# Kernel tuning notes

Hardware: AMD Instinct MI355X
Metric: run time of the kernel (lower is better)

## Reference

```python
import jax, jax.numpy as jnp
import numpy as np

NUM_QUBITS = 6
DIM = 2 ** NUM_QUBITS  # 64


def _u_gate(theta, phi, lam):
    # qiskit U(theta, phi, lam)
    c = jnp.cos(theta / 2).astype(jnp.complex64)
    s = jnp.sin(theta / 2).astype(jnp.complex64)
    ephi = jnp.exp(1j * phi.astype(jnp.complex64))
    elam = jnp.exp(1j * lam.astype(jnp.complex64))
    return jnp.stack([
        jnp.stack([c, -elam * s]),
        jnp.stack([ephi * s, ephi * elam * c]),
    ])


def _p_gate(lam):
    one = jnp.ones((), jnp.complex64)
    return jnp.stack([
        jnp.stack([one, jnp.zeros((), jnp.complex64)]),
        jnp.stack([jnp.zeros((), jnp.complex64), jnp.exp(1j * lam.astype(jnp.complex64))]),
    ])


def _controlled(U):
    # 4x4 matrix in |control, target> basis: block-diag(I2, U)
    return jnp.eye(4, dtype=jnp.complex64).at[2:, 2:].set(U)


_CX = jnp.array([[1, 0, 0, 0], [0, 1, 0, 0], [0, 0, 0, 1], [0, 0, 1, 0]], dtype=jnp.complex64)


def _apply_1q(psi, U, q):
    # psi: (B, 2,2,2,2,2,2); qubit q (qiskit little-endian) -> axis 6-q
    ax = NUM_QUBITS - q
    psi = jnp.moveaxis(psi, ax, -1)
    psi = psi @ U.T
    return jnp.moveaxis(psi, -1, ax)


def _apply_2q(psi, G, qa, qb):
    # G is 4x4 acting on (qa, qb) with index 2*bit(qa)+bit(qb)
    a, b = NUM_QUBITS - qa, NUM_QUBITS - qb
    psi = jnp.moveaxis(psi, (a, b), (-2, -1))
    shp = psi.shape
    psi = (psi.reshape(shp[:-2] + (4,)) @ G.T).reshape(shp)
    return jnp.moveaxis(psi, (-2, -1), (a, b))


def _circuit(features, params):
    # amplitude encoding (qc.initialize with L2 normalization; |0> fallback for zero vec)
    norm = jnp.linalg.norm(features, axis=1, keepdims=True)
    safe = jnp.where(jnp.isclose(norm, 0.0), 1.0, norm)
    e0 = jnp.zeros((1, DIM), features.dtype).at[0, 0].set(1.0)
    psi = jnp.where(jnp.isclose(norm, 0.0), e0, features / safe)
    psi = psi.astype(jnp.complex64).reshape((-1,) + (2,) * NUM_QUBITS)

    def U3(i):
        return _u_gate(params[i], params[i + 1], params[i + 2])

    # layer 1: U on all qubits (params 0..17)
    for q in range(NUM_QUBITS):
        psi = _apply_1q(psi, U3(3 * q), q)
    # cx(2,1); p(18,1); cx(4,3); p(19,3)
    psi = _apply_2q(psi, _CX, 2, 1)
    psi = _apply_1q(psi, _p_gate(params[18]), 1)
    psi = _apply_2q(psi, _CX, 4, 3)
    psi = _apply_1q(psi, _p_gate(params[19]), 3)
    # layer 2: U on [0,1,3,5] (params 20..31)
    idx = 20
    for q in [0, 1, 3, 5]:
        psi = _apply_1q(psi, U3(idx), q)
        idx += 3
    # controlled-U(32..34) ctrl 0 -> tgt 1; controlled-U(35..37) ctrl 3 -> tgt 5
    psi = _apply_2q(psi, _controlled(U3(32)), 0, 1)
    psi = _apply_2q(psi, _controlled(U3(35)), 3, 5)
    # cx(3,1); p(38,1)
    psi = _apply_2q(psi, _CX, 3, 1)
    psi = _apply_1q(psi, _p_gate(params[38]), 1)
    # final: U on [0,1] (39..44); CU(45..47) ctrl 0 -> tgt 1; U on [0,1] (48..53)
    psi = _apply_1q(psi, U3(39), 0)
    psi = _apply_1q(psi, U3(42), 1)
    psi = _apply_2q(psi, _controlled(U3(45)), 0, 1)
    psi = _apply_1q(psi, U3(48), 0)
    psi = _apply_1q(psi, U3(51), 1)

    # observable kron(diag(1,-1), I_32): +1 for index < 32, -1 otherwise (Z on qubit 5)
    probs = jnp.abs(psi.reshape(-1, DIM)) ** 2
    sign = jnp.where(jnp.arange(DIM) < DIM // 2, 1.0, -1.0).astype(jnp.float32)
    return (probs @ sign).astype(jnp.float32)


def setup_inputs() -> dict:
    key = jax.random.key(0)
    kf, kp = jax.random.split(key)
    features = jax.random.normal(kf, (262144, 64), dtype=jnp.float32)
    params = jax.random.uniform(kp, (54,), dtype=jnp.float32) * (0.1 * np.pi)
    return {"features": features, "params": params}


def reference(features, params):
    return _circuit(features, params)
```

## Files before the change

### kernel.cpp

```cpp
#include <hip/hip_runtime.h>
#include <hip/hip_bf16.h>

using f32x4  = __attribute__((ext_vector_type(4))) float;
using bf16x8 = __attribute__((ext_vector_type(8))) short;

__device__ __attribute__((aligned(16))) unsigned short g_Abf[64 * 64];
__device__ float2 g_U[64 * 64];
__device__ float  g_A00;

__device__ inline unsigned short f2bf(float x) {
  unsigned u = __builtin_bit_cast(unsigned, x);
  return (unsigned short)((u + 0x7FFFu + ((u >> 16) & 1u)) >> 16);
}
__device__ inline float2 cmul(float2 a, float2 b) {
  return make_float2(a.x * b.x - a.y * b.y, a.x * b.y + a.y * b.x);
}
__device__ inline float2 cadd(float2 a, float2 b) { return make_float2(a.x + b.x, a.y + b.y); }

__device__ inline void gate1q(float2* psi, int t, int sub, int q,
                              float2 u00, float2 u01, float2 u10, float2 u11) {
  const int bit = 1 << q, mask = bit - 1;
#pragma unroll
  for (int pp = 0; pp < 8; ++pp) {
    int p  = sub * 8 + pp;
    int i0 = ((p & ~mask) << 1) | (p & mask);
    int i1 = i0 | bit;
    float2 a0 = psi[i0 * 64 + t], a1 = psi[i1 * 64 + t];
    psi[i0 * 64 + t] = cadd(cmul(u00, a0), cmul(u01, a1));
    psi[i1 * 64 + t] = cadd(cmul(u10, a0), cmul(u11, a1));
  }
}

__device__ inline void gatec(float2* psi, int t, int sub, int c, int g,
                             float2 v00, float2 v01, float2 v10, float2 v11) {
  const int cb = 1 << c, gb = 1 << g;
  const int lo = (c < g ? c : g), hi = (c < g ? g : c);
  const int mlo = (1 << lo) - 1, mhi = (1 << hi) - 1;
#pragma unroll
  for (int pp = 0; pp < 4; ++pp) {
    int p = sub * 4 + pp;
    int y = ((p & ~mlo) << 1) | (p & mlo);
    y     = ((y & ~mhi) << 1) | (y & mhi);
    int i0 = y | cb;
    int i1 = i0 | gb;
    float2 a0 = psi[i0 * 64 + t], a1 = psi[i1 * 64 + t];
    psi[i0 * 64 + t] = cadd(cmul(v00, a0), cmul(v01, a1));
    psi[i1 * 64 + t] = cadd(cmul(v10, a0), cmul(v11, a1));
  }
}

__global__ __launch_bounds__(256) void sim_kernel(const float* __restrict__ P) {
  __shared__ float2 psi[64 * 64];
  __shared__ float tS[54], tC[54], tSh[54], tCh[54];
  const int t = threadIdx.x & 63, sub = threadIdx.x >> 6;
  if (threadIdx.x < 54) {
    float p = P[threadIdx.x];
    tS[threadIdx.x]  = __sinf(p);
    tC[threadIdx.x]  = __cosf(p);
    tSh[threadIdx.x] = __sinf(0.5f * p);
    tCh[threadIdx.x] = __cosf(0.5f * p);
  }
  for (int idx = threadIdx.x; idx < 4096; idx += 256)
    psi[idx] = make_float2(((idx >> 6) == (idx & 63)) ? 1.f : 0.f, 0.f);
  __syncthreads();

  float2 u00, u01, u10, u11;
  const float2 Z = make_float2(0.f, 0.f), ONE = make_float2(1.f, 0.f);
  auto U3L = [&](int i) {
    float ch = tCh[i], sh = tSh[i];
    float cp = tC[i + 1], sp = tS[i + 1];
    float cl = tC[i + 2], sl = tS[i + 2];
    u00 = make_float2(ch, 0.f);
    u01 = make_float2(-cl * sh, -sl * sh);
    u10 = make_float2(cp * sh, sp * sh);
    u11 = make_float2((cp * cl - sp * sl) * ch, (cp * sl + sp * cl) * ch);
  };
  auto PH = [&](int i) { return make_float2(tC[i], tS[i]); };

#pragma unroll
  for (int q = 0; q < 6; ++q) {
    U3L(3 * q);
    gate1q(psi, t, sub, q, u00, u01, u10, u11);
    __syncthreads();
  }
  gatec(psi, t, sub, 2, 1, Z, ONE, ONE, Z); __syncthreads();
  gate1q(psi, t, sub, 1, ONE, Z, Z, PH(18)); __syncthreads();
  gatec(psi, t, sub, 4, 3, Z, ONE, ONE, Z); __syncthreads();
  gate1q(psi, t, sub, 3, ONE, Z, Z, PH(19)); __syncthreads();
  const int qs[4] = {0, 1, 3, 5};
#pragma unroll
  for (int ii = 0; ii < 4; ++ii) {
    U3L(20 + 3 * ii);
    gate1q(psi, t, sub, qs[ii], u00, u01, u10, u11);
    __syncthreads();
  }
  U3L(32); gatec(psi, t, sub, 0, 1, u00, u01, u10, u11); __syncthreads();
  U3L(35); gatec(psi, t, sub, 3, 5, u00, u01, u10, u11); __syncthreads();
  gatec(psi, t, sub, 3, 1, Z, ONE, ONE, Z); __syncthreads();
  gate1q(psi, t, sub, 1, ONE, Z, Z, PH(38)); __syncthreads();
  U3L(39); gate1q(psi, t, sub, 0, u00, u01, u10, u11); __syncthreads();
  U3L(42); gate1q(psi, t, sub, 1, u00, u01, u10, u11); __syncthreads();
  U3L(45); gatec(psi, t, sub, 0, 1, u00, u01, u10, u11); __syncthreads();
  U3L(48); gate1q(psi, t, sub, 0, u00, u01, u10, u11); __syncthreads();
  U3L(51); gate1q(psi, t, sub, 1, u00, u01, u10, u11); __syncthreads();
  for (int idx = threadIdx.x; idx < 4096; idx += 256) g_U[idx] = psi[idx];
}

__global__ __launch_bounds__(256) void amat_kernel() {
  const int idx = blockIdx.x * 256 + threadIdx.x;
  const int j = idx >> 6, k = idx & 63;
  float s = 0.f;
#pragma unroll 8
  for (int i = 0; i < 64; ++i) {
    float2 uj = g_U[i * 64 + j], uk = g_U[i * 64 + k];
    float d = uj.x * uk.x + uj.y * uk.y;
    s += (i < 32) ? d : -d;
  }
  g_Abf[idx] = f2bf(s);
  if (idx == 0) g_A00 = s;
}

#define MFMA(A, B, C) __builtin_amdgcn_mfma_f32_16x16x32_bf16(A, B, C, 0, 0, 0)

__global__ __launch_bounds__(256) void qexp_kernel(const float* __restrict__ F, float* __restrict__ out) {
  __shared__ float flds[4][16 * 68];
  const int lane = threadIdx.x & 63;
  const int wid  = threadIdx.x >> 6;
  const int g = lane >> 4, c0 = lane & 15;
  float* fl = flds[wid];

  const unsigned short* ab = g_Abf + (unsigned)(c0 * 64 + g * 8);
  const bf16x8 b00 = *(const bf16x8*)(ab);
  const bf16x8 b01 = *(const bf16x8*)(ab + 32);
  const bf16x8 b10 = *(const bf16x8*)(ab + 16 * 64);
  const bf16x8 b11 = *(const bf16x8*)(ab + 16 * 64 + 32);
  const bf16x8 b20 = *(const bf16x8*)(ab + 32 * 64);
  const bf16x8 b21 = *(const bf16x8*)(ab + 32 * 64 + 32);
  const bf16x8 b30 = *(const bf16x8*)(ab + 48 * 64);
  const bf16x8 b31 = *(const bf16x8*)(ab + 48 * 64 + 32);
  const float A00 = g_A00;

  const int nwaves = gridDim.x << 2;
  for (int tile = (int)(blockIdx.x << 2) | wid; tile < 16384; tile += nwaves) {
    const int b0 = tile << 4;
    const float* fr = F + (size_t)(b0 + c0) * 64 + g * 8;
    const float4 v0 = *(const float4*)(fr);
    const float4 v1 = *(const float4*)(fr + 4);
    const float4 v2 = *(const float4*)(fr + 32);
    const float4 v3 = *(const float4*)(fr + 36);
    bf16x8 a0, a1;
    a0[0] = f2bf(v0.x); a0[1] = f2bf(v0.y); a0[2] = f2bf(v0.z); a0[3] = f2bf(v0.w);
    a0[4] = f2bf(v1.x); a0[5] = f2bf(v1.y); a0[6] = f2bf(v1.z); a0[7] = f2bf(v1.w);
    a1[0] = f2bf(v2.x); a1[1] = f2bf(v2.y); a1[2] = f2bf(v2.z); a1[3] = f2bf(v2.w);
    a1[4] = f2bf(v3.x); a1[5] = f2bf(v3.y); a1[6] = f2bf(v3.z); a1[7] = f2bf(v3.w);
    float* fw = fl + c0 * 68 + g * 8;
    *(float4*)(fw)      = v0;
    *(float4*)(fw + 4)  = v1;
    *(float4*)(fw + 32) = v2;
    *(float4*)(fw + 36) = v3;

    f32x4 acc0 = {0.f, 0.f, 0.f, 0.f}, acc1 = acc0, acc2 = acc0, acc3 = acc0;
    acc0 = MFMA(a0, b00, acc0); acc0 = MFMA(a1, b01, acc0);
    acc1 = MFMA(a0, b10, acc1); acc1 = MFMA(a1, b11, acc1);
    acc2 = MFMA(a0, b20, acc2); acc2 = MFMA(a1, b21, acc2);
    acc3 = MFMA(a0, b30, acc3); acc3 = MFMA(a1, b31, acc3);

    asm volatile("s_waitcnt lgkmcnt(0)" ::: "memory");
    float num0 = 0, num1 = 0, num2 = 0, num3 = 0, den0 = 0, den1 = 0, den2 = 0, den3 = 0;
    const float* fb = fl + g * 4 * 68 + c0;
#define EPI(ACC, NT) { \
    float fv0 = fb[(NT) * 16];          num0 = fmaf(ACC[0], fv0, num0); den0 = fmaf(fv0, fv0, den0); \
    float fv1 = fb[68 + (NT) * 16];     num1 = fmaf(ACC[1], fv1, num1); den1 = fmaf(fv1, fv1, den1); \
    float fv2 = fb[2 * 68 + (NT) * 16]; num2 = fmaf(ACC[2], fv2, num2); den2 = fmaf(fv2, fv2, den2); \
    float fv3 = fb[3 * 68 + (NT) * 16]; num3 = fmaf(ACC[3], fv3, num3); den3 = fmaf(fv3, fv3, den3); }
    EPI(acc0, 0) EPI(acc1, 1) EPI(acc2, 2) EPI(acc3, 3)
#undef EPI
#pragma unroll
    for (int m = 1; m < 16; m <<= 1) {
      num0 += __shfl_xor(num0, m, 64); den0 += __shfl_xor(den0, m, 64);
      num1 += __shfl_xor(num1, m, 64); den1 += __shfl_xor(den1, m, 64);
      num2 += __shfl_xor(num2, m, 64); den2 += __shfl_xor(den2, m, 64);
      num3 += __shfl_xor(num3, m, 64); den3 += __shfl_xor(den3, m, 64);
    }
    if (c0 < 4) {
      float nv = (c0 == 0) ? num0 : (c0 == 1) ? num1 : (c0 == 2) ? num2 : num3;
      float dv = (c0 == 0) ? den0 : (c0 == 1) ? den1 : (c0 == 2) ? den2 : den3;
      out[b0 + g * 4 + c0] = (dv <= 1e-16f) ? A00 : nv / dv;
    }
  }
}

extern "C" void kernel_launch(void* const* d_in, const int* in_sizes, int n_in,
                              void* d_out, int out_size, void* d_ws, size_t ws_size,
                              hipStream_t stream) {
  const float* F = (const float*)d_in[0];
  const float* P = (const float*)d_in[1];
  float* out = (float*)d_out;
  sim_kernel<<<1, 256, 0, stream>>>(P);
  amat_kernel<<<16, 256, 0, stream>>>();
  qexp_kernel<<<2048, 256, 0, stream>>>(F, out);
}
```

Measured before the change: 121.4 us.

## Fuse circuit simulation into expectation kernel, redundantly per block, using psi=Ux GEMM

Merges the three launches into one kernel. Every block re-simulates the 64x64 circuit unitary in shared memory and builds a bf16 stacked real/imag matrix of U. Each row is then handled as psi = U x via eight MFMA tiles, with the signed probability sum normalised by the total norm, instead of a quadratic form against a precomputed A matrix. A double-buffered register prefetch of feature tiles is added over 16 tiles per wave. This removes two launches and the global round trip, but each of 256 blocks repeats the serial gate simulation and the MFMA work per row doubles.

```diff
diff --git a/kernel.cpp b/kernel.cpp
--- a/kernel.cpp
+++ b/kernel.cpp
@@ -1,12 +1,7 @@
 #include <hip/hip_runtime.h>
-#include <hip/hip_bf16.h>
 
 using f32x4  = __attribute__((ext_vector_type(4))) float;
 using bf16x8 = __attribute__((ext_vector_type(8))) short;
-
-__device__ __attribute__((aligned(16))) unsigned short g_Abf[64 * 64];
-__device__ float2 g_U[64 * 64];
-__device__ float  g_A00;
 
 __device__ inline unsigned short f2bf(float x) {
   unsigned u = __builtin_bit_cast(unsigned, x);
@@ -49,18 +44,27 @@
   }
 }
 
-__global__ __launch_bounds__(256) void sim_kernel(const float* __restrict__ P) {
+#define MFMA(A, B, C) __builtin_amdgcn_mfma_f32_16x16x32_bf16(A, B, C, 0, 0, 0)
+
+__global__ __launch_bounds__(256) void qfused(const float* __restrict__ F,
+                                              const float* __restrict__ Pp,
+                                              float* __restrict__ out) {
   __shared__ float2 psi[64 * 64];
+  __shared__ __attribute__((aligned(16))) unsigned short Plds[128 * 64];
   __shared__ float tS[54], tC[54], tSh[54], tCh[54];
-  const int t = threadIdx.x & 63, sub = threadIdx.x >> 6;
-  if (threadIdx.x < 54) {
-    float p = P[threadIdx.x];
-    tS[threadIdx.x]  = __sinf(p);
-    tC[threadIdx.x]  = __cosf(p);
-    tSh[threadIdx.x] = __sinf(0.5f * p);
-    tCh[threadIdx.x] = __cosf(0.5f * p);
+  __shared__ float sA00;
+
+  const int tid = threadIdx.x;
+  const int t = tid & 63, sub = tid >> 6;
+
+  if (tid < 54) {
+    float p = Pp[tid];
+    tS[tid]  = __sinf(p);
+    tC[tid]  = __cosf(p);
+    tSh[tid] = __sinf(0.5f * p);
+    tCh[tid] = __cosf(0.5f * p);
   }
-  for (int idx = threadIdx.x; idx < 4096; idx += 256)
+  for (int idx = tid; idx < 4096; idx += 256)
     psi[idx] = make_float2(((idx >> 6) == (idx & 63)) ? 1.f : 0.f, 0.f);
   __syncthreads();
 
@@ -79,9 +83,7 @@
 
 #pragma unroll
   for (int q = 0; q < 6; ++q) {
-    U3L(3 * q);
-    gate1q(psi, t, sub, q, u00, u01, u10, u11);
-    __syncthreads();
+    U3L(3 * q); gate1q(psi, t, sub, q, u00, u01, u10, u11); __syncthreads();
   }
   gatec(psi, t, sub, 2, 1, Z, ONE, ONE, Z); __syncthreads();
   gate1q(psi, t, sub, 1, ONE, Z, Z, PH(18)); __syncthreads();
@@ -90,9 +92,7 @@
   const int qs[4] = {0, 1, 3, 5};
 #pragma unroll
   for (int ii = 0; ii < 4; ++ii) {
-    U3L(20 + 3 * ii);
-    gate1q(psi, t, sub, qs[ii], u00, u01, u10, u11);
-    __syncthreads();
+    U3L(20 + 3 * ii); gate1q(psi, t, sub, qs[ii], u00, u01, u10, u11); __syncthreads();
   }
   U3L(32); gatec(psi, t, sub, 0, 1, u00, u01, u10, u11); __syncthreads();
   U3L(35); gatec(psi, t, sub, 3, 5, u00, u01, u10, u11); __syncthreads();
@@ -103,91 +103,89 @@
   U3L(45); gatec(psi, t, sub, 0, 1, u00, u01, u10, u11); __syncthreads();
   U3L(48); gate1q(psi, t, sub, 0, u00, u01, u10, u11); __syncthreads();
   U3L(51); gate1q(psi, t, sub, 1, u00, u01, u10, u11); __syncthreads();
-  for (int idx = threadIdx.x; idx < 4096; idx += 256) g_U[idx] = psi[idx];
-}
 
-__global__ __launch_bounds__(256) void amat_kernel() {
-  const int idx = blockIdx.x * 256 + threadIdx.x;
-  const int j = idx >> 6, k = idx & 63;
-  float s = 0.f;
-#pragma unroll 8
-  for (int i = 0; i < 64; ++i) {
-    float2 uj = g_U[i * 64 + j], uk = g_U[i * 64 + k];
-    float d = uj.x * uk.x + uj.y * uk.y;
-    s += (i < 32) ? d : -d;
+  if (tid < 64) {
+    float2 v = psi[tid * 64];
+    float term = (v.x * v.x + v.y * v.y) * (tid < 32 ? 1.f : -1.f);
+#pragma unroll
+    for (int m = 1; m < 64; m <<= 1) term += __shfl_xor(term, m, 64);
+    if (tid == 0) sA00 = term;
   }
-  g_Abf[idx] = f2bf(s);
-  if (idx == 0) g_A00 = s;
-}
+  for (int idx = tid; idx < 8192; idx += 256) {
+    int r = idx >> 6, j = idx & 63;
+    int i = (r < 32) ? r : (r < 96) ? (r - 32) : (r - 64);
+    bool im = (r >= 32 && r < 64) || (r >= 96);
+    float2 v = psi[i * 64 + j];
+    Plds[idx] = f2bf(im ? v.y : v.x);
+  }
+  __syncthreads();
 
-#define MFMA(A, B, C) __builtin_amdgcn_mfma_f32_16x16x32_bf16(A, B, C, 0, 0, 0)
+  const int lane = tid & 63, wid = sub;
+  const int g = lane >> 4, c0 = lane & 15;
+  const unsigned short* pb = Plds + c0 * 64 + g * 8;
+  bf16x8 Bf[8][2];
+#pragma unroll
+  for (int nt = 0; nt < 8; ++nt) {
+    Bf[nt][0] = *(const bf16x8*)(pb + nt * 1024);
+    Bf[nt][1] = *(const bf16x8*)(pb + nt * 1024 + 32);
+  }
+  const float A00 = sA00;
 
-__global__ __launch_bounds__(256) void qexp_kernel(const float* __restrict__ F, float* __restrict__ out) {
-  __shared__ float flds[4][16 * 68];
-  const int lane = threadIdx.x & 63;
-  const int wid  = threadIdx.x >> 6;
-  const int g = lane >> 4, c0 = lane & 15;
-  float* fl = flds[wid];
+  const int tile0 = blockIdx.x * 64 + wid * 16;
+  const float* fp = F + (size_t)(tile0 * 16 + c0) * 64 + g * 8;
 
-  const unsigned short* ab = g_Abf + (unsigned)(c0 * 64 + g * 8);
-  const bf16x8 b00 = *(const bf16x8*)(ab);
-  const bf16x8 b01 = *(const bf16x8*)(ab + 32);
-  const bf16x8 b10 = *(const bf16x8*)(ab + 16 * 64);
-  const bf16x8 b11 = *(const bf16x8*)(ab + 16 * 64 + 32);
-  const bf16x8 b20 = *(const bf16x8*)(ab + 32 * 64);
-  const bf16x8 b21 = *(const bf16x8*)(ab + 32 * 64 + 32);
-  const bf16x8 b30 = *(const bf16x8*)(ab + 48 * 64);
-  const bf16x8 b31 = *(const bf16x8*)(ab + 48 * 64 + 32);
-  const float A00 = g_A00;
+#define LOADT(i, V0, V1, V2, V3) { const float* q_ = fp + (size_t)(i) * 1024; \
+    V0 = *(const float4*)(q_); V1 = *(const float4*)(q_ + 4); \
+    V2 = *(const float4*)(q_ + 32); V3 = *(const float4*)(q_ + 36); }
 
-  const int nwaves = gridDim.x << 2;
-  for (int tile = (int)(blockIdx.x << 2) | wid; tile < 16384; tile += nwaves) {
-    const int b0 = tile << 4;
-    const float* fr = F + (size_t)(b0 + c0) * 64 + g * 8;
-    const float4 v0 = *(const float4*)(fr);
-    const float4 v1 = *(const float4*)(fr + 4);
-    const float4 v2 = *(const float4*)(fr + 32);
-    const float4 v3 = *(const float4*)(fr + 36);
-    bf16x8 a0, a1;
-    a0[0] = f2bf(v0.x); a0[1] = f2bf(v0.y); a0[2] = f2bf(v0.z); a0[3] = f2bf(v0.w);
-    a0[4] = f2bf(v1.x); a0[5] = f2bf(v1.y); a0[6] = f2bf(v1.z); a0[7] = f2bf(v1.w);
-    a1[0] = f2bf(v2.x); a1[1] = f2bf(v2.y); a1[2] = f2bf(v2.z); a1[3] = f2bf(v2.w);
-    a1[4] = f2bf(v3.x); a1[5] = f2bf(v3.y); a1[6] = f2bf(v3.z); a1[7] = f2bf(v3.w);
-    float* fw = fl + c0 * 68 + g * 8;
-    *(float4*)(fw)      = v0;
-    *(float4*)(fw + 4)  = v1;
-    *(float4*)(fw + 32) = v2;
-    *(float4*)(fw + 36) = v3;
+#define PROCESS(i, V0, V1, V2, V3) { \
+    bf16x8 a0, a1; \
+    a0[0] = f2bf(V0.x); a0[1] = f2bf(V0.y); a0[2] = f2bf(V0.z); a0[3] = f2bf(V0.w); \
+    a0[4] = f2bf(V1.x); a0[5] = f2bf(V1.y); a0[6] = f2bf(V1.z); a0[7] = f2bf(V1.w); \
+    a1[0] = f2bf(V2.x); a1[1] = f2bf(V2.y); a1[2] = f2bf(V2.z); a1[3] = f2bf(V2.w); \
+    a1[4] = f2bf(V3.x); a1[5] = f2bf(V3.y); a1[6] = f2bf(V3.z); a1[7] = f2bf(V3.w); \
+    f32x4 acc[8]; \
+    _Pragma("unroll") \
+    for (int nt = 0; nt < 8; ++nt) { \
+      acc[nt] = (f32x4){0.f, 0.f, 0.f, 0.f}; \
+      acc[nt] = MFMA(a0, Bf[nt][0], acc[nt]); \
+      acc[nt] = MFMA(a1, Bf[nt][1], acc[nt]); \
+    } \
+    float s1[4] = {0, 0, 0, 0}, s2[4] = {0, 0, 0, 0}; \
+    _Pragma("unroll") \
+    for (int nt = 0; nt < 4; ++nt) { \
+      _Pragma("unroll") \
+      for (int r = 0; r < 4; ++r) { \
+        s1[r] = fmaf(acc[nt][r], acc[nt][r], s1[r]); \
+        s2[r] = fmaf(acc[nt + 4][r], acc[nt + 4][r], s2[r]); \
+      } \
+    } \
+    _Pragma("unroll") \
+    for (int m = 1; m < 16; m <<= 1) { \
+      _Pragma("unroll") \
+      for (int r = 0; r < 4; ++r) { \
+        s1[r] += __shfl_xor(s1[r], m, 64); \
+        s2[r] += __shfl_xor(s2[r], m, 64); \
+      } \
+    } \
+    if (c0 < 4) { \
+      float sp_ = (c0 == 0) ? s1[0] : (c0 == 1) ? s1[1] : (c0 == 2) ? s1[2] : s1[3]; \
+      float sm_ = (c0 == 0) ? s2[0] : (c0 == 1) ? s2[1] : (c0 == 2) ? s2[2] : s2[3]; \
+      float den = sp_ + sm_; \
+      out[(size_t)(tile0 + (i)) * 16 + 4 * g + c0] = (den < 1e-30f) ? A00 : (sp_ - sm_) / den; \
+    } }
 
-    f32x4 acc0 = {0.f, 0.f, 0.f, 0.f}, acc1 = acc0, acc2 = acc0, acc3 = acc0;
-    acc0 = MFMA(a0, b00, acc0); acc0 = MFMA(a1, b01, acc0);
-    acc1 = MFMA(a0, b10, acc1); acc1 = MFMA(a1, b11, acc1);
-    acc2 = MFMA(a0, b20, acc2); acc2 = MFMA(a1, b21, acc2);
-    acc3 = MFMA(a0, b30, acc3); acc3 = MFMA(a1, b31, acc3);
-
-    asm volatile("s_waitcnt lgkmcnt(0)" ::: "memory");
-    float num0 = 0, num1 = 0, num2 = 0, num3 = 0, den0 = 0, den1 = 0, den2 = 0, den3 = 0;
-    const float* fb = fl + g * 4 * 68 + c0;
-#define EPI(ACC, NT) { \
-    float fv0 = fb[(NT) * 16];          num0 = fmaf(ACC[0], fv0, num0); den0 = fmaf(fv0, fv0, den0); \
-    float fv1 = fb[68 + (NT) * 16];     num1 = fmaf(ACC[1], fv1, num1); den1 = fmaf(fv1, fv1, den1); \
-    float fv2 = fb[2 * 68 + (NT) * 16]; num2 = fmaf(ACC[2], fv2, num2); den2 = fmaf(fv2, fv2, den2); \
-    float fv3 = fb[3 * 68 + (NT) * 16]; num3 = fmaf(ACC[3], fv3, num3); den3 = fmaf(fv3, fv3, den3); }
-    EPI(acc0, 0) EPI(acc1, 1) EPI(acc2, 2) EPI(acc3, 3)
-#undef EPI
+  float4 x0, x1, x2, x3, y0, y1, y2, y3;
+  LOADT(0, x0, x1, x2, x3);
 #pragma unroll
-    for (int m = 1; m < 16; m <<= 1) {
-      num0 += __shfl_xor(num0, m, 64); den0 += __shfl_xor(den0, m, 64);
-      num1 += __shfl_xor(num1, m, 64); den1 += __shfl_xor(den1, m, 64);
-      num2 += __shfl_xor(num2, m, 64); den2 += __shfl_xor(den2, m, 64);
-      num3 += __shfl_xor(num3, m, 64); den3 += __shfl_xor(den3, m, 64);
-    }
-    if (c0 < 4) {
-      float nv = (c0 == 0) ? num0 : (c0 == 1) ? num1 : (c0 == 2) ? num2 : num3;
-      float dv = (c0 == 0) ? den0 : (c0 == 1) ? den1 : (c0 == 2) ? den2 : den3;
-      out[b0 + g * 4 + c0] = (dv <= 1e-16f) ? A00 : nv / dv;
-    }
+  for (int i = 0; i < 16; i += 2) {
+    LOADT(i + 1, y0, y1, y2, y3);
+    PROCESS(i, x0, x1, x2, x3);
+    if (i + 2 < 16) LOADT(i + 2, x0, x1, x2, x3);
+    PROCESS(i + 1, y0, y1, y2, y3);
   }
+#undef LOADT
+#undef PROCESS
 }
 
 extern "C" void kernel_launch(void* const* d_in, const int* in_sizes, int n_in,
@@ -196,7 +194,5 @@
   const float* F = (const float*)d_in[0];
   const float* P = (const float*)d_in[1];
   float* out = (float*)d_out;
-  sim_kernel<<<1, 256, 0, stream>>>(P);
-  amat_kernel<<<16, 256, 0, stream>>>();
-  qexp_kernel<<<2048, 256, 0, stream>>>(F, out);
+  qfused<<<256, 256, 0, stream>>>(F, P, out);
 }
```

New measurement: 120.0 us. Within noise of the previous version (-1.1%).
